# Performance work log

Measured on AMD Instinct MI355X. Metric: run time of the kernel, lower is better.

## Reference

```python
import jax, jax.numpy as jnp
import numpy as np
from jax import lax

FACTOR = 2          # upsample factor
PAD = (2, 1)        # ((pad+1)//2 + factor - 1, pad//2) with pad = k_len - factor = 2


def setup_inputs() -> dict:
    key = jax.random.key(0)
    x = jax.random.normal(key, (16, 256, 64, 64), dtype=jnp.float32)  # NCHW feature map
    # make_kernel([1,3,3,1]) * factor**2
    k1 = jnp.array([1.0, 3.0, 3.0, 1.0], dtype=jnp.float32)
    k = k1[None, :] * k1[:, None]          # 4x4 separable FIR kernel
    k = k / jnp.sum(k) * (FACTOR ** 2)
    return {"x": x, "kernel": k}


def reference(x, kernel):
    """upfirdn2d(x, kernel, up=FACTOR, down=1, pad=PAD).

    Fused zero-insert upsample + pad + FIR conv, expressed as a single
    depthwise lax.conv_general_dilated with lhs_dilation (no materialized
    zero-stuffed intermediate).
    """
    B, C, H, W = x.shape
    up = FACTOR
    pad0, pad1 = PAD
    # upfirdn convolves (not correlates) with the kernel -> flip for XLA's correlation.
    k = jnp.flip(kernel)[None, None]               # (1, 1, kh, kw)
    k = jnp.tile(k, (C, 1, 1, 1))                  # depthwise weights, OIHW
    # XLA lhs_dilation yields size (H-1)*up+1; the reference zero-insertion yields
    # H*up (with up-1 trailing zeros), so fold those trailing zeros into pad1.
    pads = [(pad0, pad1 + up - 1), (pad0, pad1 + up - 1)]
    out = lax.conv_general_dilated(
        x, k,
        window_strides=(1, 1),
        padding=pads,
        lhs_dilation=(up, up),
        feature_group_count=C,
        dimension_numbers=("NCHW", "OIHW", "NCHW"))
    return out  # (B, C, H*up, W*up)
```

## Files before the change

kernel.cpp:

```cpp
#include <hip/hip_runtime.h>


#define H_IN  64
#define W_IN  64
#define H_OUT 128
#define W_OUT 128

__global__ __launch_bounds__(256) void upsample_2x_kernel(
    const float* __restrict__ x, float* __restrict__ out, int total) {
  int idx = blockIdx.x * 256 + threadIdx.x;
  if (idx >= total) return;

  int q   = idx & 31;
  int r   = (idx >> 5) & 63;
  int img = idx >> 11;

  const float* xi = x + (size_t)img * (H_IN * W_IN);
  float*       oi = out + (size_t)img * (H_OUT * W_OUT);

  const int c = 2 * q;

  float v[3][4];
#pragma unroll
  for (int i = 0; i < 3; ++i) {
    int row = r - 1 + i;
    bool rok = (row >= 0) & (row < H_IN);
    const float* xr = xi + row * W_IN;
    float2 m = rok ? *(const float2*)(xr + c) : make_float2(0.f, 0.f);
    v[i][1] = m.x;
    v[i][2] = m.y;
    v[i][0] = (rok && q != 0)  ? xr[c - 1] : 0.f;
    v[i][3] = (rok && q != 31) ? xr[c + 2] : 0.f;
  }

  float h[3][4];
#pragma unroll
  for (int i = 0; i < 3; ++i) {
    h[i][0] = 0.25f * v[i][0] + 0.75f * v[i][1];
    h[i][1] = 0.75f * v[i][1] + 0.25f * v[i][2];
    h[i][2] = 0.25f * v[i][1] + 0.75f * v[i][2];
    h[i][3] = 0.75f * v[i][2] + 0.25f * v[i][3];
  }

  float4 o0, o1;
  o0.x = 0.25f * h[0][0] + 0.75f * h[1][0];
  o0.y = 0.25f * h[0][1] + 0.75f * h[1][1];
  o0.z = 0.25f * h[0][2] + 0.75f * h[1][2];
  o0.w = 0.25f * h[0][3] + 0.75f * h[1][3];
  o1.x = 0.75f * h[1][0] + 0.25f * h[2][0];
  o1.y = 0.75f * h[1][1] + 0.25f * h[2][1];
  o1.z = 0.75f * h[1][2] + 0.25f * h[2][2];
  o1.w = 0.75f * h[1][3] + 0.25f * h[2][3];

  float* orow0 = oi + (2 * r) * W_OUT + 4 * q;
  float* orow1 = orow0 + W_OUT;
  *(float4*)orow0 = o0;
  *(float4*)orow1 = o1;
}

extern "C" void kernel_launch(void* const* d_in, const int* in_sizes, int n_in,
                              void* d_out, int out_size, void* d_ws, size_t ws_size,
                              hipStream_t stream) {
  const float* x = (const float*)d_in[0];
  float* out = (float*)d_out;
  const int total = 16 * 256 * 64 * 32;
  const int blocks = total / 256;
  upsample_2x_kernel<<<blocks, 256, 0, stream>>>(x, out, total);
}
```

Before: 342.4 us.

## Compute four output rows per thread and share halo columns via wave shuffles

Each thread now handles two input rows and writes four output rows, so it loads four input rows instead of three rows for every one input row. This cuts redundant global reads between neighbouring threads. The scalar loads of left and right halo columns are replaced with __shfl_up/__shfl_down between lanes, zeroed at row edges. The grid is halved, which gives more work per thread but fewer threads in flight.

```diff
diff --git a/kernel.cpp b/kernel.cpp
--- a/kernel.cpp
+++ b/kernel.cpp
@@ -1,61 +1,64 @@
 #include <hip/hip_runtime.h>
 
 
-#define H_IN  64
-#define W_IN  64
-#define H_OUT 128
-#define W_OUT 128
+__global__ __launch_bounds__(256) void upsample_2x_kernel(
+    const float* __restrict__ x, float* __restrict__ out) {
+  int idx = blockIdx.x * 256 + threadIdx.x;
+  int q   = idx & 31;
+  int t   = (idx >> 5) & 31;
+  int img = idx >> 10;
 
-__global__ __launch_bounds__(256) void upsample_2x_kernel(
-    const float* __restrict__ x, float* __restrict__ out, int total) {
-  int idx = blockIdx.x * 256 + threadIdx.x;
-  if (idx >= total) return;
+  const float* xi = x + (size_t)img * (64 * 64);
+  float*       oi = out + (size_t)img * (128 * 128);
 
-  int q   = idx & 31;
-  int r   = (idx >> 5) & 63;
-  int img = idx >> 11;
+  const int c  = 2 * q;
+  const int r0 = 2 * t;
 
-  const float* xi = x + (size_t)img * (H_IN * W_IN);
-  float*       oi = out + (size_t)img * (H_OUT * W_OUT);
+  float2 m[4];
+  m[0] = (t > 0)  ? *(const float2*)(xi + (r0 - 1) * 64 + c) : make_float2(0.f, 0.f);
+  m[1] =            *(const float2*)(xi + (r0    ) * 64 + c);
+  m[2] =            *(const float2*)(xi + (r0 + 1) * 64 + c);
+  m[3] = (t < 31) ? *(const float2*)(xi + (r0 + 2) * 64 + c) : make_float2(0.f, 0.f);
 
-  const int c = 2 * q;
-
-  float v[3][4];
+  float h[4][4];
 #pragma unroll
-  for (int i = 0; i < 3; ++i) {
-    int row = r - 1 + i;
-    bool rok = (row >= 0) & (row < H_IN);
-    const float* xr = xi + row * W_IN;
-    float2 m = rok ? *(const float2*)(xr + c) : make_float2(0.f, 0.f);
-    v[i][1] = m.x;
-    v[i][2] = m.y;
-    v[i][0] = (rok && q != 0)  ? xr[c - 1] : 0.f;
-    v[i][3] = (rok && q != 31) ? xr[c + 2] : 0.f;
+  for (int i = 0; i < 4; ++i) {
+    float left  = __shfl_up(m[i].y, 1);
+    float right = __shfl_down(m[i].x, 1);
+    if (q == 0)  left  = 0.f;
+    if (q == 31) right = 0.f;
+    h[i][0] = 0.25f * left   + 0.75f * m[i].x;
+    h[i][1] = 0.75f * m[i].x + 0.25f * m[i].y;
+    h[i][2] = 0.25f * m[i].x + 0.75f * m[i].y;
+    h[i][3] = 0.75f * m[i].y + 0.25f * right;
   }
 
-  float h[3][4];
-#pragma unroll
-  for (int i = 0; i < 3; ++i) {
-    h[i][0] = 0.25f * v[i][0] + 0.75f * v[i][1];
-    h[i][1] = 0.75f * v[i][1] + 0.25f * v[i][2];
-    h[i][2] = 0.25f * v[i][1] + 0.75f * v[i][2];
-    h[i][3] = 0.75f * v[i][2] + 0.25f * v[i][3];
-  }
+  float* op = oi + (4 * t) * 128 + 4 * q;
+  float4 o;
 
-  float4 o0, o1;
-  o0.x = 0.25f * h[0][0] + 0.75f * h[1][0];
-  o0.y = 0.25f * h[0][1] + 0.75f * h[1][1];
-  o0.z = 0.25f * h[0][2] + 0.75f * h[1][2];
-  o0.w = 0.25f * h[0][3] + 0.75f * h[1][3];
-  o1.x = 0.75f * h[1][0] + 0.25f * h[2][0];
-  o1.y = 0.75f * h[1][1] + 0.25f * h[2][1];
-  o1.z = 0.75f * h[1][2] + 0.25f * h[2][2];
-  o1.w = 0.75f * h[1][3] + 0.25f * h[2][3];
+  o.x = 0.25f * h[0][0] + 0.75f * h[1][0];
+  o.y = 0.25f * h[0][1] + 0.75f * h[1][1];
+  o.z = 0.25f * h[0][2] + 0.75f * h[1][2];
+  o.w = 0.25f * h[0][3] + 0.75f * h[1][3];
+  *(float4*)(op) = o;
 
-  float* orow0 = oi + (2 * r) * W_OUT + 4 * q;
-  float* orow1 = orow0 + W_OUT;
-  *(float4*)orow0 = o0;
-  *(float4*)orow1 = o1;
+  o.x = 0.75f * h[1][0] + 0.25f * h[2][0];
+  o.y = 0.75f * h[1][1] + 0.25f * h[2][1];
+  o.z = 0.75f * h[1][2] + 0.25f * h[2][2];
+  o.w = 0.75f * h[1][3] + 0.25f * h[2][3];
+  *(float4*)(op + 128) = o;
+
+  o.x = 0.25f * h[1][0] + 0.75f * h[2][0];
+  o.y = 0.25f * h[1][1] + 0.75f * h[2][1];
+  o.z = 0.25f * h[1][2] + 0.75f * h[2][2];
+  o.w = 0.25f * h[1][3] + 0.75f * h[2][3];
+  *(float4*)(op + 256) = o;
+
+  o.x = 0.75f * h[2][0] + 0.25f * h[3][0];
+  o.y = 0.75f * h[2][1] + 0.25f * h[3][1];
+  o.z = 0.75f * h[2][2] + 0.25f * h[3][2];
+  o.w = 0.75f * h[2][3] + 0.25f * h[3][3];
+  *(float4*)(op + 384) = o;
 }
 
 extern "C" void kernel_launch(void* const* d_in, const int* in_sizes, int n_in,
@@ -63,7 +66,6 @@
                               hipStream_t stream) {
   const float* x = (const float*)d_in[0];
   float* out = (float*)d_out;
-  const int total = 16 * 256 * 64 * 32;
-  const int blocks = total / 256;
-  upsample_2x_kernel<<<blocks, 256, 0, stream>>>(x, out, total);
+  const int blocks = (16 * 256 * 32 * 32) / 256;
+  upsample_2x_kernel<<<blocks, 256, 0, stream>>>(x, out);
 }
```

Measured after the change: 310.5 us. 9.3% less time.
